# Kernel optimization log

Measured on AMD Instinct MI355X. Metric: run time of the kernel, lower is better.

Reference implementation:

```python
import jax, jax.numpy as jnp
import numpy as np

N, E, B = 80000, 480000, 800  # nodes, edges, graphs
H, C = 4, 64                  # attention heads, per-head channels

def gelu(x):
    return jax.nn.gelu(x, approximate=False)

def setup_inputs() -> dict:
    key = jax.random.key(0)
    ks = jax.random.split(key, 40)
    nrm = lambda k, shp, s=0.1: jax.random.normal(k, shp, jnp.float32) * s
    inp = {
        'x': jax.random.normal(ks[0], (N, 21), jnp.float32),
        'edge_index': jax.random.randint(ks[1], (2, E), 0, N, dtype=jnp.int32),
        'batch_idx': jnp.sort(jax.random.randint(ks[2], (N,), 0, B, dtype=jnp.int32)),
        'rnafm': jax.random.normal(ks[3], (B, 640), jnp.float32),
        'hand_feat': jax.random.normal(ks[4], (B, 40), jnp.float32),
        # GATConv params: lin weight [H*C, in], att_src/att_dst [H, C], bias [C]
        'g1_W': nrm(ks[5], (H * C, 21)), 'g1_as': nrm(ks[6], (H, C)), 'g1_ad': nrm(ks[7], (H, C)), 'g1_b': nrm(ks[8], (C,)),
        'g2_W': nrm(ks[9], (H * C, C)), 'g2_as': nrm(ks[10], (H, C)), 'g2_ad': nrm(ks[11], (H, C)), 'g2_b': nrm(ks[12], (C,)),
        'g3_W': nrm(ks[13], (H * C, C)), 'g3_as': nrm(ks[14], (H, C)), 'g3_ad': nrm(ks[15], (H, C)), 'g3_b': nrm(ks[16], (C,)),
        'pool_W': nrm(ks[17], (1, C)), 'pool_b': nrm(ks[18], (1,)),
        'e1_W': nrm(ks[19], (256, 744)), 'e1_b': nrm(ks[20], (256,)),
        'ln_g': jnp.ones((256,), jnp.float32), 'ln_b': jnp.zeros((256,), jnp.float32),
        'e2_W': nrm(ks[21], (128, 256)), 'e2_b': nrm(ks[22], (128,)),
        'bin_W': nrm(ks[23], (1, 128)), 'bin_b': nrm(ks[24], (1,)),
        'ad1_W': nrm(ks[25], (5, 32, 128)), 'ad1_b': nrm(ks[26], (5, 32)),
        'ad2_W': nrm(ks[27], (5, 1, 32)), 'ad2_b': nrm(ks[28], (5, 1)),
        'c1_W': nrm(ks[29], (64, 128)), 'c1_b': nrm(ks[30], (64,)),
        'c2_W': nrm(ks[31], (6, 64)), 'c2_b': nrm(ks[32], (6,)),
    }
    return inp


def reference(x, edge_index, batch_idx, rnafm, hand_feat,
              g1_W, g1_as, g1_ad, g1_b,
              g2_W, g2_as, g2_ad, g2_b,
              g3_W, g3_as, g3_ad, g3_b,
              pool_W, pool_b, e1_W, e1_b, ln_g, ln_b, e2_W, e2_b,
              bin_W, bin_b, ad1_W, ad1_b, ad2_W, ad2_b, c1_W, c1_b, c2_W, c2_b):
    n = x.shape[0]
    # PyG GATConv default: add self loops
    loops = jnp.arange(n, dtype=edge_index.dtype)
    ei = jnp.concatenate([edge_index, jnp.stack([loops, loops])], axis=1)
    src, dst = ei[0], ei[1]

    def gat(h_in, W, a_s, a_d, b):
        h = (h_in @ W.T).reshape(n, H, C)              # [N,H,C]
        s = (h * a_s[None]).sum(-1)                    # [N,H] att_src . h
        d = (h * a_d[None]).sum(-1)                    # [N,H]
        e = jax.nn.leaky_relu(s[src] + d[dst], 0.2)    # [E',H]
        m = jax.ops.segment_max(e, dst, num_segments=n)
        ex = jnp.exp(e - m[dst])                       # segment softmax (stable)
        z = jax.ops.segment_sum(ex, dst, num_segments=n)
        alpha = ex / z[dst]                            # [E',H]
        out = jax.ops.segment_sum(h[src] * alpha[:, :, None], dst, num_segments=n)
        return out.mean(axis=1) + b                    # concat=False -> mean heads

    h = gelu(gat(x, g1_W, g1_as, g1_ad, g1_b))
    h = gelu(gat(h, g2_W, g2_as, g2_ad, g2_b))
    h = gelu(gat(h, g3_W, g3_as, g3_ad, g3_b))

    # attention-weighted pooling; softmax over ALL nodes (dim=0), as in source
    attn = jax.nn.softmax(h @ pool_W.T + pool_b, axis=0)   # [N,1]
    pooled = jax.ops.segment_sum(h * attn, batch_idx, num_segments=B)  # [B,64]

    fused = jnp.concatenate([pooled, rnafm, hand_feat], axis=-1)       # [B,744]
    z1 = gelu(fused @ e1_W.T + e1_b)
    mu = z1.mean(-1, keepdims=True)
    var = ((z1 - mu) ** 2).mean(-1, keepdims=True)
    z1 = (z1 - mu) / jnp.sqrt(var + 1e-5) * ln_g + ln_b
    shared = gelu(z1 @ e2_W.T + e2_b)                      # [B,128]

    binary = (shared @ bin_W.T + bin_b)[:, 0]              # [B]
    h1 = gelu(jnp.einsum('bd,ehd->ebh', shared, ad1_W) + ad1_b[:, None, :])
    per = jnp.einsum('ebh,eh->eb', h1, ad2_W[:, 0, :]) + ad2_b  # [5,B]
    cls = gelu(shared @ c1_W.T + c1_b) @ c2_W.T + c2_b     # [B,6]
    return binary, per, cls
```

## Files before the change

kernel.cpp:

```cpp
#include <hip/hip_runtime.h>
#include <hip/hip_bf16.h>
#include <math.h>

constexpr int N_NODES = 80000;
constexpr int N_EDGES = 480000;
constexpr int N_B     = 800;
constexpr int PADDEG  = 64;

typedef __attribute__((ext_vector_type(8))) short bf16x8;
typedef __attribute__((ext_vector_type(4))) float f32x4;

__device__ __forceinline__ float gelu_exact(float x) {
    return 0.5f * x * (1.0f + erff(x * 0.70710678118654752f));
}
__device__ __forceinline__ float lrelu(float v) {
    return v > 0.f ? v : 0.2f * v;
}
__device__ __forceinline__ unsigned short f2bf(float f) {
    unsigned u = __float_as_uint(f);
    unsigned r = u + 0x7FFFu + ((u >> 16) & 1u);
    return (unsigned short)(r >> 16);
}
__device__ __forceinline__ float bf2f(unsigned short h) {
    return __uint_as_float(((unsigned)h) << 16);
}

template<int IN_DIM>
__launch_bounds__(256, 2)
__global__ void gat_transform(const float* __restrict__ xin,
                              const float* __restrict__ W,
                              const float* __restrict__ aS,
                              const float* __restrict__ aD,
                              unsigned short* __restrict__ hfull,
                              float* __restrict__ sArr,
                              float* __restrict__ dArr) {
    constexpr int K  = (IN_DIM + 31) & ~31;
    constexpr int KS = K / 32;
    constexpr int KP = K + 8;
    __shared__ __align__(16) unsigned short Wb[256 * KP];
    __shared__ __align__(16) unsigned short xs[32 * KP];

    const int tid = threadIdx.x;
    const int lane = tid & 63, w = tid >> 6;

    for (int idx = tid; idx < 256 * K; idx += 256) {
        int c = idx / K, k = idx - c * K;
        Wb[c * KP + k] = (k < IN_DIM) ? f2bf(W[c * IN_DIM + k]) : (unsigned short)0;
    }
    __syncthreads();

    bf16x8 bfrag[4][KS];
    float asv[4], adv[4];
#pragma unroll
    for (int t = 0; t < 4; ++t) {
        const int ch = w * 64 + t * 16 + (lane & 15);
#pragma unroll
        for (int s = 0; s < KS; ++s)
            bfrag[t][s] = *reinterpret_cast<const bf16x8*>(&Wb[ch * KP + s * 32 + (lane >> 4) * 8]);
        asv[t] = aS[ch];
        adv[t] = aD[ch];
    }

    const int ntiles = N_NODES / 32;
    for (int tile = blockIdx.x; tile < ntiles; tile += gridDim.x) {
        const int n0 = tile * 32;
        __syncthreads();
        for (int idx = tid; idx < 32 * K; idx += 256) {
            int r = idx / K, k = idx - r * K;
            xs[r * KP + k] = (k < IN_DIM) ? f2bf(xin[(size_t)(n0 + r) * IN_DIM + k])
                                          : (unsigned short)0;
        }
        __syncthreads();

        f32x4 acc[2][4];
#pragma unroll
        for (int m = 0; m < 2; ++m) {
            bf16x8 afrag[KS];
#pragma unroll
            for (int s = 0; s < KS; ++s)
                afrag[s] = *reinterpret_cast<const bf16x8*>(
                    &xs[(m * 16 + (lane & 15)) * KP + s * 32 + (lane >> 4) * 8]);
#pragma unroll
            for (int t = 0; t < 4; ++t) {
                f32x4 a = {0.f, 0.f, 0.f, 0.f};
#pragma unroll
                for (int s = 0; s < KS; ++s)
                    a = __builtin_amdgcn_mfma_f32_16x16x32_bf16(afrag[s], bfrag[t][s], a, 0, 0, 0);
                acc[m][t] = a;
            }
        }

#pragma unroll
        for (int m = 0; m < 2; ++m) {
            float sv[4] = {0, 0, 0, 0}, dv[4] = {0, 0, 0, 0};
#pragma unroll
            for (int t = 0; t < 4; ++t) {
                const int ch = w * 64 + t * 16 + (lane & 15);
#pragma unroll
                for (int j = 0; j < 4; ++j) {
                    float hv = acc[m][t][j];
                    int node = n0 + m * 16 + (lane >> 4) * 4 + j;
                    hfull[(size_t)node * 256 + ch] = f2bf(hv);
                    sv[j] += hv * asv[t];
                    dv[j] += hv * adv[t];
                }
            }
#pragma unroll
            for (int j = 0; j < 4; ++j) {
                sv[j] += __shfl_xor(sv[j], 1, 64); dv[j] += __shfl_xor(dv[j], 1, 64);
                sv[j] += __shfl_xor(sv[j], 2, 64); dv[j] += __shfl_xor(dv[j], 2, 64);
                sv[j] += __shfl_xor(sv[j], 4, 64); dv[j] += __shfl_xor(dv[j], 4, 64);
                sv[j] += __shfl_xor(sv[j], 8, 64); dv[j] += __shfl_xor(dv[j], 8, 64);
                if ((lane & 15) == 0) {
                    int node = n0 + m * 16 + (lane >> 4) * 4 + j;
                    sArr[node * 4 + w] = sv[j];
                    dArr[node * 4 + w] = dv[j];
                }
            }
        }
    }
}

__global__ void csr_scatter_pad(const int* __restrict__ ei,
                                int* __restrict__ cnt, int* __restrict__ csrc) {
    int e = blockIdx.x * 256 + threadIdx.x;
    if (e >= N_EDGES) return;
    int src = ei[e], dst = ei[N_EDGES + e];
    int slot = atomicAdd(&cnt[dst], 1);
    csrc[(size_t)dst * PADDEG + slot] = src;
}

template<bool POOL>
__launch_bounds__(256)
__global__ void gat_gather(const int* __restrict__ cnt, const int* __restrict__ csrc,
                           const float* __restrict__ sArr, const float* __restrict__ dArr,
                           const unsigned short* __restrict__ hfull,
                           const float* __restrict__ bias,
                           const float* __restrict__ poolW, const float* __restrict__ poolB,
                           float* __restrict__ xout,
                           float* __restrict__ logit, float* __restrict__ pmax) {
    constexpr int CAP = PADDEG;
    __shared__ float qbuf[4][2][CAP * 4];
    __shared__ int   sbuf[4][2][CAP];
    __shared__ float xbuf[4][2][64];
    __shared__ float red[8];

    const int wid = threadIdx.x >> 6;
    const int lane = threadIdx.x & 63;
    const int nl = lane >> 5;
    const int sub = lane & 31;
    const int n = blockIdx.x * 8 + wid * 2 + nl;

    const int jb = n * PADDEG;
    const int deg = cnt[n];

    const int hh = sub & 3;
    const int slot = sub >> 2;
    const float dv = dArr[n * 4 + hh];
    const float qself = expf(lrelu(sArr[n * 4 + hh] + dv));
    float zp = 0.f;

    for (int base = 0; base < deg; base += 8) {
        int s = base + slot;
        if (s < deg) {
            int src = csrc[jb + s];
            float q = expf(lrelu(sArr[src * 4 + hh] + dv));
            qbuf[wid][nl][s * 4 + hh] = q;
            if (hh == 0) sbuf[wid][nl][s] = src;
            zp += q;
        }
    }
    zp += __shfl_xor(zp, 4, 64);
    zp += __shfl_xor(zp, 8, 64);
    zp += __shfl_xor(zp, 16, 64);
    const float inv = 0.25f / (zp + qself);
    __threadfence_block();

    const int h = sub >> 3;
    const int c8 = sub * 8;
    const int bl = (lane & 32) + h;
    const float inv_g = __shfl(inv, bl, 64);
    const float qs_g  = __shfl(qself, bl, 64);

#define LOADU4(S) (*reinterpret_cast<const uint4*>(&hfull[(size_t)(unsigned)(S) * 256 + c8]))
#define UNPK_FMA(A, Q, U) { \
    A[0] = fmaf((Q), __uint_as_float((U).x << 16),          A[0]); \
    A[1] = fmaf((Q), __uint_as_float((U).x & 0xFFFF0000u),  A[1]); \
    A[2] = fmaf((Q), __uint_as_float((U).y << 16),          A[2]); \
    A[3] = fmaf((Q), __uint_as_float((U).y & 0xFFFF0000u),  A[3]); \
    A[4] = fmaf((Q), __uint_as_float((U).z << 16),          A[4]); \
    A[5] = fmaf((Q), __uint_as_float((U).z & 0xFFFF0000u),  A[5]); \
    A[6] = fmaf((Q), __uint_as_float((U).w << 16),          A[6]); \
    A[7] = fmaf((Q), __uint_as_float((U).w & 0xFFFF0000u),  A[7]); }

    float accA[8] = {0, 0, 0, 0, 0, 0, 0, 0};
    float accB[8] = {0, 0, 0, 0, 0, 0, 0, 0};
    {
        uint4 us = LOADU4(n);
        UNPK_FMA(accA, qs_g, us);
    }
    int s = 0;
    for (; s + 1 < deg; s += 2) {
        int s0 = sbuf[wid][nl][s], s1 = sbuf[wid][nl][s + 1];
        float q0 = qbuf[wid][nl][s * 4 + h];
        float q1 = qbuf[wid][nl][(s + 1) * 4 + h];
        uint4 u0 = LOADU4(s0);
        uint4 u1 = LOADU4(s1);
        UNPK_FMA(accA, q0, u0);
        UNPK_FMA(accB, q1, u1);
    }
    if (s < deg) {
        int s0 = sbuf[wid][nl][s];
        float q0 = qbuf[wid][nl][s * 4 + h];
        uint4 u0 = LOADU4(s0);
        UNPK_FMA(accA, q0, u0);
    }
#undef UNPK_FMA
#undef LOADU4

    float acc[8];
#pragma unroll
    for (int j = 0; j < 8; ++j) acc[j] = (accA[j] + accB[j]) * inv_g;

#pragma unroll
    for (int j = 0; j < 8; ++j) {
        acc[j] += __shfl_xor(acc[j], 8, 64);
        acc[j] += __shfl_xor(acc[j], 16, 64);
    }

    {
        float w0 = (h == 0) ? acc[0] : (h == 1) ? acc[2] : (h == 2) ? acc[4] : acc[6];
        float w1 = (h == 0) ? acc[1] : (h == 1) ? acc[3] : (h == 2) ? acc[5] : acc[7];
        const int rc = (sub & 7) * 8 + h * 2;
        xbuf[wid][nl][rc]     = w0;
        xbuf[wid][nl][rc + 1] = w1;
    }
    __threadfence_block();

    const int c2 = sub * 2;
    float o0 = gelu_exact(xbuf[wid][nl][c2]     + bias[c2]);
    float o1 = gelu_exact(xbuf[wid][nl][c2 + 1] + bias[c2 + 1]);
    *reinterpret_cast<float2*>(&xout[(size_t)n * 64 + c2]) = make_float2(o0, o1);

    if (POOL) {
        float p = o0 * poolW[c2] + o1 * poolW[c2 + 1];
#pragma unroll
        for (int of = 1; of < 32; of <<= 1) p += __shfl_xor(p, of, 64);
        float lg = p + poolB[0];
        if (sub == 0) {
            logit[n] = lg;
            red[wid * 2 + nl] = lg;
        }
        __syncthreads();
        if (threadIdx.x == 0) {
            float mm = red[0];
#pragma unroll
            for (int i = 1; i < 8; ++i) mm = fmaxf(mm, red[i]);
            pmax[blockIdx.x] = mm;
        }
    }
}

__global__ void reduce_max(const float* __restrict__ pmax, int n,
                           float* __restrict__ gmax) {
    __shared__ float red[256];
    float m = -INFINITY;
    for (int i = threadIdx.x; i < n; i += 256) m = fmaxf(m, pmax[i]);
    red[threadIdx.x] = m;
    __syncthreads();
    for (int s = 128; s > 0; s >>= 1) {
        if (threadIdx.x < s) red[threadIdx.x] = fmaxf(red[threadIdx.x], red[threadIdx.x + s]);
        __syncthreads();
    }
    if (threadIdx.x == 0) *gmax = red[0];
}

__global__ void seg_bounds(const int* __restrict__ batch, int* __restrict__ start) {
    int n = blockIdx.x * 256 + threadIdx.x;
    if (n >= N_NODES) return;
    int b1 = batch[n];
    int b0 = (n == 0) ? -1 : batch[n - 1];
    for (int b = b0 + 1; b <= b1; ++b) start[b] = n;
    if (n == N_NODES - 1)
        for (int b = b1 + 1; b <= N_B; ++b) start[b] = N_NODES;
}

__global__ void pool_graph(const float* __restrict__ h3,
                           const float* __restrict__ logit,
                           const float* __restrict__ gmax,
                           const int* __restrict__ start,
                           float* __restrict__ pooled,
                           float* __restrict__ gsum) {
    __shared__ float sacc[4][64];
    __shared__ float sw[4];
    int b = blockIdx.x;
    int s = start[b], e = start[b + 1];
    int lane = threadIdx.x & 63, wid = threadIdx.x >> 6;
    float M = *gmax;
    float acc = 0.f, wsum = 0.f;
    for (int n = s + wid; n < e; n += 4) {
        float w = expf(logit[n] - M);
        acc += h3[(size_t)n * 64 + lane] * w;
        if (lane == 0) wsum += w;
    }
    sacc[wid][lane] = acc;
    if (lane == 0) sw[wid] = wsum;
    __syncthreads();
    if (wid == 0) {
        pooled[(size_t)b * 64 + lane] = sacc[0][lane] + sacc[1][lane] + sacc[2][lane] + sacc[3][lane];
        if (lane == 0) atomicAdd(gsum, sw[0] + sw[1] + sw[2] + sw[3]);
    }
}

constexpr int GB1  = 8;
constexpr int KSEG = 372;

__launch_bounds__(256, 4)
__global__ void head1_part(const float* __restrict__ pooled, const float* __restrict__ gsum,
                           const float* __restrict__ rnafm, const float* __restrict__ hand,
                           const float* __restrict__ e1W,
                           float* __restrict__ part) {
    __shared__ __align__(16) float fused[GB1][KSEG + 4];
    const int bq = blockIdx.x >> 1;
    const int ks = blockIdx.x & 1;
    const int g0 = bq * GB1;
    const int k0 = ks * KSEG;
    const int tid = threadIdx.x;
    const float inv = 1.0f / *gsum;

    for (int idx = tid; idx < GB1 * KSEG; idx += 256) {
        int g = idx / KSEG, kk = idx - g * KSEG;
        int k = kk + k0;
        int b = g0 + g;
        float v;
        if (k < 64)       v = pooled[(size_t)b * 64 + k] * inv;
        else if (k < 704) v = rnafm[(size_t)b * 640 + (k - 64)];
        else              v = hand[(size_t)b * 40 + (k - 704)];
        fused[g][kk] = v;
    }
    __syncthreads();

    const float* wr = e1W + (size_t)tid * 744 + k0;
    float a0 = 0.f, a1 = 0.f, a2 = 0.f, a3 = 0.f;
    float a4 = 0.f, a5 = 0.f, a6 = 0.f, a7 = 0.f;
    for (int q = 0; q < KSEG / 4; ++q) {
        float4 w4 = *reinterpret_cast<const float4*>(wr + q * 4);
        float4 f0 = *reinterpret_cast<const float4*>(&fused[0][q * 4]);
        float4 f1 = *reinterpret_cast<const float4*>(&fused[1][q * 4]);
        float4 f2 = *reinterpret_cast<const float4*>(&fused[2][q * 4]);
        float4 f3 = *reinterpret_cast<const float4*>(&fused[3][q * 4]);
        float4 f4 = *reinterpret_cast<const float4*>(&fused[4][q * 4]);
        float4 f5 = *reinterpret_cast<const float4*>(&fused[5][q * 4]);
        float4 f6 = *reinterpret_cast<const float4*>(&fused[6][q * 4]);
        float4 f7 = *reinterpret_cast<const float4*>(&fused[7][q * 4]);
        a0 += f0.x * w4.x + f0.y * w4.y + f0.z * w4.z + f0.w * w4.w;
        a1 += f1.x * w4.x + f1.y * w4.y + f1.z * w4.z + f1.w * w4.w;
        a2 += f2.x * w4.x + f2.y * w4.y + f2.z * w4.z + f2.w * w4.w;
        a3 += f3.x * w4.x + f3.y * w4.y + f3.z * w4.z + f3.w * w4.w;
        a4 += f4.x * w4.x + f4.y * w4.y + f4.z * w4.z + f4.w * w4.w;
        a5 += f5.x * w4.x + f5.y * w4.y + f5.z * w4.z + f5.w * w4.w;
        a6 += f6.x * w4.x + f6.y * w4.y + f6.z * w4.z + f6.w * w4.w;
        a7 += f7.x * w4.x + f7.y * w4.y + f7.z * w4.z + f7.w * w4.w;
    }
    float* po = part + ((size_t)ks * N_B + g0) * 256 + tid;
    po[0 * 256] = a0; po[1 * 256] = a1; po[2 * 256] = a2; po[3 * 256] = a3;
    po[4 * 256] = a4; po[5 * 256] = a5; po[6 * 256] = a6; po[7 * 256] = a7;
}

__launch_bounds__(256, 2)
__global__ void head_fused(const float* __restrict__ part,
                           const float* __restrict__ e1b,
                           const float* __restrict__ lng, const float* __restrict__ lnb,
                           const float* __restrict__ e2W, const float* __restrict__ e2b,
                           const float* __restrict__ binW, const float* __restrict__ binB,
                           const float* __restrict__ ad1W, const float* __restrict__ ad1b,
                           const float* __restrict__ ad2W, const float* __restrict__ ad2b,
                           const float* __restrict__ c1W, const float* __restrict__ c1b,
                           const float* __restrict__ c2W, const float* __restrict__ c2b,
                           float* __restrict__ out) {
    __shared__ float zr[4][256];
    __shared__ float red1[4][4], red2[4][4];
    __shared__ float sv[4][128];
    __shared__ float t64[4][64];
    __shared__ float h1s[4][5][32];
    __shared__ float binred[4][32];
    const int b0 = blockIdx.x * 4;
    const int tid = threadIdx.x;
    const int lane = tid & 63, wid = tid >> 6;

    const float eb = e1b[tid];
    float g0 = gelu_exact(part[(size_t)(b0 + 0) * 256 + tid] + part[((size_t)N_B + b0 + 0) * 256 + tid] + eb);
    float g1 = gelu_exact(part[(size_t)(b0 + 1) * 256 + tid] + part[((size_t)N_B + b0 + 1) * 256 + tid] + eb);
    float g2 = gelu_exact(part[(size_t)(b0 + 2) * 256 + tid] + part[((size_t)N_B + b0 + 2) * 256 + tid] + eb);
    float g3 = gelu_exact(part[(size_t)(b0 + 3) * 256 + tid] + part[((size_t)N_B + b0 + 3) * 256 + tid] + eb);

    float s10 = g0, s11 = g1, s12 = g2, s13 = g3;
    float s20 = g0 * g0, s21 = g1 * g1, s22 = g2 * g2, s23 = g3 * g3;
#pragma unroll
    for (int o = 1; o < 64; o <<= 1) {
        s10 += __shfl_xor(s10, o, 64); s11 += __shfl_xor(s11, o, 64);
        s12 += __shfl_xor(s12, o, 64); s13 += __shfl_xor(s13, o, 64);
        s20 += __shfl_xor(s20, o, 64); s21 += __shfl_xor(s21, o, 64);
        s22 += __shfl_xor(s22, o, 64); s23 += __shfl_xor(s23, o, 64);
    }
    if (lane == 0) {
        red1[wid][0] = s10; red1[wid][1] = s11; red1[wid][2] = s12; red1[wid][3] = s13;
        red2[wid][0] = s20; red2[wid][1] = s21; red2[wid][2] = s22; red2[wid][3] = s23;
    }
    __syncthreads();

    const float gN = lng[tid], bN = lnb[tid];
#pragma unroll
    for (int bb = 0; bb < 4; ++bb) {
        float s1 = red1[0][bb] + red1[1][bb] + red1[2][bb] + red1[3][bb];
        float s2 = red2[0][bb] + red2[1][bb] + red2[2][bb] + red2[3][bb];
        float mu  = s1 * (1.0f / 256.0f);
        float var = s2 * (1.0f / 256.0f) - mu * mu;
        float g = (bb == 0) ? g0 : (bb == 1) ? g1 : (bb == 2) ? g2 : g3;
        zr[bb][tid] = (g - mu) * rsqrtf(var + 1e-5f) * gN + bN;
    }
    __syncthreads();

    {
        const int ch = tid & 127, gp = tid >> 7;
        const float* wr = e2W + (size_t)ch * 256;
        const float e2bb = e2b[ch];
        float a0 = e2bb, a1 = e2bb;
        for (int k = 0; k < 256; k += 4) {
            float4 w4 = *reinterpret_cast<const float4*>(wr + k);
            float4 f0 = *reinterpret_cast<const float4*>(&zr[gp * 2][k]);
            float4 f1 = *reinterpret_cast<const float4*>(&zr[gp * 2 + 1][k]);
            a0 += f0.x * w4.x + f0.y * w4.y + f0.z * w4.z + f0.w * w4.w;
            a1 += f1.x * w4.x + f1.y * w4.y + f1.z * w4.z + f1.w * w4.w;
        }
        sv[gp * 2][ch]     = gelu_exact(a0);
        sv[gp * 2 + 1][ch] = gelu_exact(a1);
    }
    __syncthreads();

    for (int idx = tid; idx < 256 + 640; idx += 256) {
        if (idx < 256) {
            int g = idx >> 6, ch = idx & 63;
            float a = c1b[ch];
            const float* wr = c1W + (size_t)ch * 128;
            for (int k = 0; k < 128; ++k) a += sv[g][k] * wr[k];
            t64[g][ch] = gelu_exact(a);
        } else {
            int j = idx - 256;
            int g = j / 160, r = j - g * 160;
            int e = r >> 5, hh = r & 31;
            float a = ad1b[e * 32 + hh];
            const float* wr = ad1W + (size_t)(e * 32 + hh) * 128;
            for (int k = 0; k < 128; ++k) a += sv[g][k] * wr[k];
            h1s[g][e][hh] = gelu_exact(a);
        }
    }
    if (tid < 128) {
        int g = tid >> 5, r = tid & 31;
        float a = 0.f;
#pragma unroll
        for (int k = 0; k < 4; ++k) a += sv[g][r * 4 + k] * binW[r * 4 + k];
        binred[g][r] = a;
    }
    __syncthreads();

    if (tid < 24) {
        int g = tid / 6, c = tid - g * 6;
        float a = c2b[c];
        const float* wr = c2W + (size_t)c * 64;
        for (int k = 0; k < 64; ++k) a += t64[g][k] * wr[k];
        out[4800 + (size_t)(b0 + g) * 6 + c] = a;
    }
    if (tid >= 32 && tid < 52) {
        int j = tid - 32;
        int g = j / 5, e = j - g * 5;
        float a = ad2b[e];
        const float* wr = ad2W + (size_t)e * 32;
        for (int k = 0; k < 32; ++k) a += h1s[g][e][k] * wr[k];
        out[800 + (size_t)e * 800 + (b0 + g)] = a;
    }
    if (tid >= 64 && tid < 68) {
        int g = tid - 64;
        float a = binB[0];
        for (int r = 0; r < 32; ++r) a += binred[g][r];
        out[b0 + g] = a;
    }
}

extern "C" void kernel_launch(void* const* d_in, const int* in_sizes, int n_in,
                              void* d_out, int out_size, void* d_ws, size_t ws_size,
                              hipStream_t stream) {
    const float* x       = (const float*)d_in[0];
    const int*   ei      = (const int*)d_in[1];
    const int*   batch   = (const int*)d_in[2];
    const float* rnafm   = (const float*)d_in[3];
    const float* hand    = (const float*)d_in[4];
    const float* gW[3]  = {(const float*)d_in[5],  (const float*)d_in[9],  (const float*)d_in[13]};
    const float* gAs[3] = {(const float*)d_in[6],  (const float*)d_in[10], (const float*)d_in[14]};
    const float* gAd[3] = {(const float*)d_in[7],  (const float*)d_in[11], (const float*)d_in[15]};
    const float* gB[3]  = {(const float*)d_in[8],  (const float*)d_in[12], (const float*)d_in[16]};
    const float* poolW = (const float*)d_in[17];
    const float* poolB = (const float*)d_in[18];
    const float* e1W = (const float*)d_in[19]; const float* e1b = (const float*)d_in[20];
    const float* lng = (const float*)d_in[21]; const float* lnb = (const float*)d_in[22];
    const float* e2W = (const float*)d_in[23]; const float* e2b = (const float*)d_in[24];
    const float* binW = (const float*)d_in[25]; const float* binB = (const float*)d_in[26];
    const float* ad1W = (const float*)d_in[27]; const float* ad1b = (const float*)d_in[28];
    const float* ad2W = (const float*)d_in[29]; const float* ad2b = (const float*)d_in[30];
    const float* c1W = (const float*)d_in[31]; const float* c1b = (const float*)d_in[32];
    const float* c2W = (const float*)d_in[33]; const float* c2b = (const float*)d_in[34];
    float* out = (float*)d_out;

    float* ws = (float*)d_ws;
    size_t off = 0;
    unsigned short* hfull = (unsigned short*)(ws + off); off += (size_t)N_NODES * 128;
    float* xcur   = ws + off; off += (size_t)N_NODES * 64;
    float* sArr   = ws + off; off += (size_t)N_NODES * 4;
    float* dArr   = ws + off; off += (size_t)N_NODES * 4;
    int*   cnt    = (int*)(ws + off); off += N_NODES;
    int*   csrc   = (int*)(ws + off); off += (size_t)N_NODES * PADDEG;
    float* logit  = ws + off; off += N_NODES;
    float* pmax   = ws + off; off += 20000;
    float* pooled = ws + off; off += (size_t)N_B * 64;
    float* part   = ws + off; off += (size_t)2 * N_B * 256;
    int*   start  = (int*)(ws + off); off += (N_B + 1);
    float* gmax   = ws + off; off += 1;
    float* gsum   = ws + off; off += 1;

    hipMemsetAsync(cnt, 0, N_NODES * sizeof(int), stream);
    csr_scatter_pad<<<(N_EDGES + 255) / 256, 256, 0, stream>>>(ei, cnt, csrc);
    seg_bounds<<<(N_NODES + 255) / 256, 256, 0, stream>>>(batch, start);

    for (int layer = 0; layer < 3; ++layer) {
        const float* xin = (layer == 0) ? x : xcur;
        if (layer == 0)
            gat_transform<21><<<512, 256, 0, stream>>>(xin, gW[0], gAs[0], gAd[0], hfull, sArr, dArr);
        else
            gat_transform<64><<<512, 256, 0, stream>>>(xin, gW[layer], gAs[layer], gAd[layer], hfull, sArr, dArr);
        if (layer < 2)
            gat_gather<false><<<N_NODES / 8, 256, 0, stream>>>(cnt, csrc, sArr, dArr, hfull,
                                                               gB[layer], nullptr, nullptr,
                                                               xcur, nullptr, nullptr);
        else
            gat_gather<true><<<N_NODES / 8, 256, 0, stream>>>(cnt, csrc, sArr, dArr, hfull,
                                                              gB[2], poolW, poolB,
                                                              xcur, logit, pmax);
    }

    reduce_max<<<1, 256, 0, stream>>>(pmax, N_NODES / 8, gmax);
    hipMemsetAsync(gsum, 0, sizeof(float), stream);
    pool_graph<<<N_B, 256, 0, stream>>>(xcur, logit, gmax, start, pooled, gsum);

    head1_part<<<(N_B / GB1) * 2, 256, 0, stream>>>(pooled, gsum, rnafm, hand, e1W, part);
    head_fused<<<N_B / 4, 256, 0, stream>>>(part, e1b, lng, lnb, e2W, e2b,
                                            binW, binB, ad1W, ad1b, ad2W, ad2b,
                                            c1W, c1b, c2W, c2b, out);
}
```

Baseline: 355.5 us.

## Process four nodes per wavefront in GAT gather with 16 columns per lane

```diff
diff --git a/kernel.cpp b/kernel.cpp
--- a/kernel.cpp
+++ b/kernel.cpp
@@ -140,16 +140,15 @@
                            float* __restrict__ xout,
                            float* __restrict__ logit, float* __restrict__ pmax) {
     constexpr int CAP = PADDEG;
-    __shared__ float qbuf[4][2][CAP * 4];
-    __shared__ int   sbuf[4][2][CAP];
-    __shared__ float xbuf[4][2][64];
-    __shared__ float red[8];
+    __shared__ float qbuf[4][4][CAP * 4];
+    __shared__ int   sbuf[4][4][CAP];
+    __shared__ float red[16];
 
     const int wid = threadIdx.x >> 6;
     const int lane = threadIdx.x & 63;
-    const int nl = lane >> 5;
-    const int sub = lane & 31;
-    const int n = blockIdx.x * 8 + wid * 2 + nl;
+    const int nl = lane >> 4;
+    const int sub = lane & 15;
+    const int n = blockIdx.x * 16 + wid * 4 + nl;
 
     const int jb = n * PADDEG;
     const int deg = cnt[n];
@@ -160,7 +159,7 @@
     const float qself = expf(lrelu(sArr[n * 4 + hh] + dv));
     float zp = 0.f;
 
-    for (int base = 0; base < deg; base += 8) {
+    for (int base = 0; base < deg; base += 4) {
         int s = base + slot;
         if (s < deg) {
             int src = csrc[jb + s];
@@ -172,90 +171,95 @@
     }
     zp += __shfl_xor(zp, 4, 64);
     zp += __shfl_xor(zp, 8, 64);
-    zp += __shfl_xor(zp, 16, 64);
     const float inv = 0.25f / (zp + qself);
     __threadfence_block();
 
-    const int h = sub >> 3;
-    const int c8 = sub * 8;
-    const int bl = (lane & 32) + h;
+    const int h = sub >> 2;
+    const int c16 = sub * 16;
+    const int bl = (lane & 48) + h;
     const float inv_g = __shfl(inv, bl, 64);
     const float qs_g  = __shfl(qself, bl, 64);
 
-#define LOADU4(S) (*reinterpret_cast<const uint4*>(&hfull[(size_t)(unsigned)(S) * 256 + c8]))
-#define UNPK_FMA(A, Q, U) { \
-    A[0] = fmaf((Q), __uint_as_float((U).x << 16),          A[0]); \
-    A[1] = fmaf((Q), __uint_as_float((U).x & 0xFFFF0000u),  A[1]); \
-    A[2] = fmaf((Q), __uint_as_float((U).y << 16),          A[2]); \
-    A[3] = fmaf((Q), __uint_as_float((U).y & 0xFFFF0000u),  A[3]); \
-    A[4] = fmaf((Q), __uint_as_float((U).z << 16),          A[4]); \
-    A[5] = fmaf((Q), __uint_as_float((U).z & 0xFFFF0000u),  A[5]); \
-    A[6] = fmaf((Q), __uint_as_float((U).w << 16),          A[6]); \
-    A[7] = fmaf((Q), __uint_as_float((U).w & 0xFFFF0000u),  A[7]); }
-
-    float accA[8] = {0, 0, 0, 0, 0, 0, 0, 0};
-    float accB[8] = {0, 0, 0, 0, 0, 0, 0, 0};
+#define LOADU4(S, C) (*reinterpret_cast<const uint4*>(&hfull[(size_t)(unsigned)(S) * 256 + (C)]))
+#define UNPK8(A, B, Q, U) { \
+    A[B + 0] = fmaf((Q), __uint_as_float((U).x << 16),          A[B + 0]); \
+    A[B + 1] = fmaf((Q), __uint_as_float((U).x & 0xFFFF0000u),  A[B + 1]); \
+    A[B + 2] = fmaf((Q), __uint_as_float((U).y << 16),          A[B + 2]); \
+    A[B + 3] = fmaf((Q), __uint_as_float((U).y & 0xFFFF0000u),  A[B + 3]); \
+    A[B + 4] = fmaf((Q), __uint_as_float((U).z << 16),          A[B + 4]); \
+    A[B + 5] = fmaf((Q), __uint_as_float((U).z & 0xFFFF0000u),  A[B + 5]); \
+    A[B + 6] = fmaf((Q), __uint_as_float((U).w << 16),          A[B + 6]); \
+    A[B + 7] = fmaf((Q), __uint_as_float((U).w & 0xFFFF0000u),  A[B + 7]); }
+
+    float acc[16] = {0, 0, 0, 0, 0, 0, 0, 0, 0, 0, 0, 0, 0, 0, 0, 0};
     {
-        uint4 us = LOADU4(n);
-        UNPK_FMA(accA, qs_g, us);
+        uint4 ua = LOADU4(n, c16);
+        uint4 ub = LOADU4(n, c16 + 8);
+        UNPK8(acc, 0, qs_g, ua);
+        UNPK8(acc, 8, qs_g, ub);
     }
     int s = 0;
     for (; s + 1 < deg; s += 2) {
         int s0 = sbuf[wid][nl][s], s1 = sbuf[wid][nl][s + 1];
         float q0 = qbuf[wid][nl][s * 4 + h];
         float q1 = qbuf[wid][nl][(s + 1) * 4 + h];
-        uint4 u0 = LOADU4(s0);
-        uint4 u1 = LOADU4(s1);
-        UNPK_FMA(accA, q0, u0);
-        UNPK_FMA(accB, q1, u1);
+        uint4 u0a = LOADU4(s0, c16);
+        uint4 u0b = LOADU4(s0, c16 + 8);
+        uint4 u1a = LOADU4(s1, c16);
+        uint4 u1b = LOADU4(s1, c16 + 8);
+        UNPK8(acc, 0, q0, u0a);
+        UNPK8(acc, 8, q0, u0b);
+        UNPK8(acc, 0, q1, u1a);
+        UNPK8(acc, 8, q1, u1b);
     }
     if (s < deg) {
         int s0 = sbuf[wid][nl][s];
         float q0 = qbuf[wid][nl][s * 4 + h];
-        uint4 u0 = LOADU4(s0);
-        UNPK_FMA(accA, q0, u0);
-    }
-#undef UNPK_FMA
+        uint4 u0a = LOADU4(s0, c16);
+        uint4 u0b = LOADU4(s0, c16 + 8);
+        UNPK8(acc, 0, q0, u0a);
+        UNPK8(acc, 8, q0, u0b);
+    }
+#undef UNPK8
 #undef LOADU4
 
-    float acc[8];
-#pragma unroll
-    for (int j = 0; j < 8; ++j) acc[j] = (accA[j] + accB[j]) * inv_g;
-
-#pragma unroll
-    for (int j = 0; j < 8; ++j) {
+#pragma unroll
+    for (int j = 0; j < 16; ++j) acc[j] *= inv_g;
+#pragma unroll
+    for (int j = 0; j < 16; ++j) {
+        acc[j] += __shfl_xor(acc[j], 4, 64);
         acc[j] += __shfl_xor(acc[j], 8, 64);
-        acc[j] += __shfl_xor(acc[j], 16, 64);
-    }
-
-    {
-        float w0 = (h == 0) ? acc[0] : (h == 1) ? acc[2] : (h == 2) ? acc[4] : acc[6];
-        float w1 = (h == 0) ? acc[1] : (h == 1) ? acc[3] : (h == 2) ? acc[5] : acc[7];
-        const int rc = (sub & 7) * 8 + h * 2;
-        xbuf[wid][nl][rc]     = w0;
-        xbuf[wid][nl][rc + 1] = w1;
-    }
-    __threadfence_block();
-
-    const int c2 = sub * 2;
-    float o0 = gelu_exact(xbuf[wid][nl][c2]     + bias[c2]);
-    float o1 = gelu_exact(xbuf[wid][nl][c2 + 1] + bias[c2 + 1]);
-    *reinterpret_cast<float2*>(&xout[(size_t)n * 64 + c2]) = make_float2(o0, o1);
+    }
+
+    const int qq = sub & 3;
+    const int cc = qq * 16 + h * 4;
+    float v0 = (h == 0) ? acc[0] : (h == 1) ? acc[4] : (h == 2) ? acc[8]  : acc[12];
+    float v1 = (h == 0) ? acc[1] : (h == 1) ? acc[5] : (h == 2) ? acc[9]  : acc[13];
+    float v2 = (h == 0) ? acc[2] : (h == 1) ? acc[6] : (h == 2) ? acc[10] : acc[14];
+    float v3 = (h == 0) ? acc[3] : (h == 1) ? acc[7] : (h == 2) ? acc[11] : acc[15];
+    const float4 b4 = *reinterpret_cast<const float4*>(&bias[cc]);
+    float4 o4;
+    o4.x = gelu_exact(v0 + b4.x);
+    o4.y = gelu_exact(v1 + b4.y);
+    o4.z = gelu_exact(v2 + b4.z);
+    o4.w = gelu_exact(v3 + b4.w);
+    *reinterpret_cast<float4*>(&xout[(size_t)n * 64 + cc]) = o4;
 
     if (POOL) {
-        float p = o0 * poolW[c2] + o1 * poolW[c2 + 1];
-#pragma unroll
-        for (int of = 1; of < 32; of <<= 1) p += __shfl_xor(p, of, 64);
+        const float4 pw = *reinterpret_cast<const float4*>(&poolW[cc]);
+        float p = o4.x * pw.x + o4.y * pw.y + o4.z * pw.z + o4.w * pw.w;
+#pragma unroll
+        for (int of = 1; of < 16; of <<= 1) p += __shfl_xor(p, of, 64);
         float lg = p + poolB[0];
         if (sub == 0) {
             logit[n] = lg;
-            red[wid * 2 + nl] = lg;
+            red[wid * 4 + nl] = lg;
         }
         __syncthreads();
         if (threadIdx.x == 0) {
             float mm = red[0];
 #pragma unroll
-            for (int i = 1; i < 8; ++i) mm = fmaxf(mm, red[i]);
+            for (int i = 1; i < 16; ++i) mm = fmaxf(mm, red[i]);
             pmax[blockIdx.x] = mm;
         }
     }
@@ -538,16 +542,16 @@
         else
             gat_transform<64><<<512, 256, 0, stream>>>(xin, gW[layer], gAs[layer], gAd[layer], hfull, sArr, dArr);
         if (layer < 2)
-            gat_gather<false><<<N_NODES / 8, 256, 0, stream>>>(cnt, csrc, sArr, dArr, hfull,
-                                                               gB[layer], nullptr, nullptr,
-                                                               xcur, nullptr, nullptr);
+            gat_gather<false><<<N_NODES / 16, 256, 0, stream>>>(cnt, csrc, sArr, dArr, hfull,
+                                                                gB[layer], nullptr, nullptr,
+                                                                xcur, nullptr, nullptr);
         else
-            gat_gather<true><<<N_NODES / 8, 256, 0, stream>>>(cnt, csrc, sArr, dArr, hfull,
-                                                              gB[2], poolW, poolB,
-                                                              xcur, logit, pmax);
-    }
-
-    reduce_max<<<1, 256, 0, stream>>>(pmax, N_NODES / 8, gmax);
+            gat_gather<true><<<N_NODES / 16, 256, 0, stream>>>(cnt, csrc, sArr, dArr, hfull,
+                                                               gB[2], poolW, poolB,
+                                                               xcur, logit, pmax);
+    }
+
+    reduce_max<<<1, 256, 0, stream>>>(pmax, N_NODES / 16, gmax);
     hipMemsetAsync(gsum, 0, sizeof(float), stream);
     pool_graph<<<N_B, 256, 0, stream>>>(xcur, logit, gmax, start, pooled, gsum);
 
```

Result: no change. 354.1 us (-0.4%).
